# Kernel optimization log

Hardware: AMD Instinct MI355X
Metric: run time of the kernel (lower is better)

The kernel has to match this reference:

```python
import jax, jax.numpy as jnp
import numpy as np

HID = 64; N_LAYERS = 4; N_HEADS = 4; HEAD_DIM = 16; INTER = 32; MAXP = 1024; EPS = 1e-12


def setup_inputs() -> dict:
    key = jax.random.key(0)
    ks = iter(jax.random.split(key, 32))
    rn = lambda shape, s=0.02: jax.random.normal(next(ks), shape, jnp.float32) * s
    B, L = 32, 1024
    return {
        "features": jax.random.normal(next(ks), (B, L, HID), jnp.float32),
        "Wq": rn((N_LAYERS, HID, HID)), "bq": jnp.zeros((N_LAYERS, HID), jnp.float32),
        "Wk": rn((N_LAYERS, HID, HID)), "bk": jnp.zeros((N_LAYERS, HID), jnp.float32),
        "Wv": rn((N_LAYERS, HID, HID)), "bv": jnp.zeros((N_LAYERS, HID), jnp.float32),
        "Wo": rn((N_LAYERS, HID, HID)), "bo": jnp.zeros((N_LAYERS, HID), jnp.float32),
        "ln1_g": jnp.ones((N_LAYERS, HID), jnp.float32), "ln1_b": jnp.zeros((N_LAYERS, HID), jnp.float32),
        "Wi": rn((N_LAYERS, HID, INTER)), "bi": jnp.zeros((N_LAYERS, INTER), jnp.float32),
        "Wd": rn((N_LAYERS, INTER, HID)), "bd": jnp.zeros((N_LAYERS, HID), jnp.float32),
        "ln2_g": jnp.ones((N_LAYERS, HID), jnp.float32), "ln2_b": jnp.zeros((N_LAYERS, HID), jnp.float32),
        "rel_emb": rn((N_LAYERS, 2 * MAXP - 1, HEAD_DIM)),
        "fc_w": rn((HID, 6)), "fc_b": jnp.zeros((6,), jnp.float32),
    }


def _ln(x, g, b):
    m = jnp.mean(x, axis=-1, keepdims=True)
    v = jnp.mean((x - m) ** 2, axis=-1, keepdims=True)
    return (x - m) / jnp.sqrt(v + EPS) * g + b


def reference(features, Wq, bq, Wk, bk, Wv, bv, Wo, bo, ln1_g, ln1_b,
              Wi, bi, Wd, bd, ln2_g, ln2_b, rel_emb, fc_w, fc_b):
    B, L, _ = features.shape
    pos = jnp.arange(L)
    dist_idx = pos[:, None] - pos[None, :] + (MAXP - 1)  # [L, L] in [0, 2*MAXP-2]
    scale = np.float32(1.0 / np.sqrt(HEAD_DIM))

    def heads(t):  # [B,L,HID] -> [B,H,L,D]
        return t.reshape(B, L, N_HEADS, HEAD_DIM).transpose(0, 2, 1, 3)

    x = features
    for i in range(N_LAYERS):
        q = heads(x @ Wq[i] + bq[i])
        k = heads(x @ Wk[i] + bk[i])
        v = heads(x @ Wv[i] + bv[i])
        scores = jnp.einsum("bhld,bhrd->bhlr", q, k)
        pe = rel_emb[i][dist_idx]  # [L, L, D] relative_key positional embedding
        scores = scores + jnp.einsum("bhld,lrd->bhlr", q, pe)
        probs = jax.nn.softmax(scores * scale, axis=-1)
        ctx = jnp.einsum("bhlr,bhrd->bhld", probs, v).transpose(0, 2, 1, 3).reshape(B, L, HID)
        x = _ln(ctx @ Wo[i] + bo[i] + x, ln1_g[i], ln1_b[i])
        inter = jax.nn.gelu(x @ Wi[i] + bi[i], approximate=False)
        x = _ln(inter @ Wd[i] + bd[i] + x, ln2_g[i], ln2_b[i])
    return (x @ fc_w + fc_b)[:, 1:, :]
```

## Files before the change

### kernel.cpp

```cpp
#include <hip/hip_runtime.h>
#include <math.h>

static constexpr int Bc = 32;
static constexpr int Lc = 1024;

typedef _Float16 f16x4 __attribute__((ext_vector_type(4)));
typedef __fp16   h16x2 __attribute__((ext_vector_type(2)));
typedef float    f32x4 __attribute__((ext_vector_type(4)));

#define MFMA16(a, b, c) __builtin_amdgcn_mfma_f32_16x16x16f16((a), (b), (c), 0, 0, 0)

#if __has_builtin(__builtin_amdgcn_exp2f)
#define EXP2(x) __builtin_amdgcn_exp2f(x)
#else
#define EXP2(x) exp2f(x)
#endif

__global__ __launch_bounds__(256) void prep_kernel(
    const float* __restrict__ features, const float* __restrict__ rel,
    const float* __restrict__ Wq, const float* __restrict__ Wk,
    const float* __restrict__ Wv, const float* __restrict__ Wo,
    const float* __restrict__ Wi, const float* __restrict__ Wd,
    _Float16* __restrict__ xh, _Float16* __restrict__ relh,
    _Float16* __restrict__ wt)
{
    int i = blockIdx.x * 256 + threadIdx.x;
    {
        float4 v = ((const float4*)features)[i];
        h16x2 a = __builtin_amdgcn_cvt_pkrtz(v.x, v.y);
        h16x2 b = __builtin_amdgcn_cvt_pkrtz(v.z, v.w);
        f16x4 o; o[0] = a[0]; o[1] = a[1]; o[2] = b[0]; o[3] = b[1];
        ((f16x4*)xh)[i] = o;
    }
    if (i < 32752) {
        float4 v = ((const float4*)rel)[i];
        h16x2 a = __builtin_amdgcn_cvt_pkrtz(v.x, v.y);
        h16x2 b = __builtin_amdgcn_cvt_pkrtz(v.z, v.w);
        f16x4 o; o[0] = a[0]; o[1] = a[1]; o[2] = b[0]; o[3] = b[1];
        ((f16x4*)relh)[i] = o;
    }
    if (i < 65536) {
        int which = i >> 14, r = i & 16383;
        int m = r >> 12, k = (r >> 6) & 63, c = r & 63;
        const float* src = which == 0 ? Wq : which == 1 ? Wk : which == 2 ? Wv : Wo;
        wt[which * 16384 + m * 4096 + c * 64 + k] = (_Float16)src[r];
    } else if (i < 73728) {
        int r = i - 65536;
        int m = r >> 11, k = (r >> 5) & 63, c = r & 31;
        wt[65536 + m * 2048 + c * 64 + k] = (_Float16)Wi[r];
    } else if (i < 81920) {
        int r = i - 73728;
        int m = r >> 11, k = (r >> 6) & 31, c = r & 63;
        wt[73728 + m * 2048 + c * 32 + k] = (_Float16)Wd[r];
    }
}

__global__ __launch_bounds__(256) void qkv_kernel(
    const _Float16* __restrict__ xh,
    const _Float16* __restrict__ qT, const _Float16* __restrict__ kT,
    const _Float16* __restrict__ vT,
    const float* __restrict__ bq, const float* __restrict__ bk,
    const float* __restrict__ bv,
    _Float16* __restrict__ qo, _Float16* __restrict__ ko, _Float16* __restrict__ vt)
{
    const int t = threadIdx.x, wv = t >> 6, lane = t & 63, lo = lane & 15, hi = lane >> 4;
    const int row0 = blockIdx.x * 64 + wv * 16;
    const int b = row0 >> 10, l0 = row0 & 1023;

    f16x4 a[4];
    #pragma unroll
    for (int kk = 0; kk < 4; kk++)
        a[kk] = *(const f16x4*)(xh + (row0 + lo) * 64 + kk * 16 + 4 * hi);

    #pragma unroll
    for (int m = 0; m < 3; m++) {
        const _Float16* WT = m == 0 ? qT : m == 1 ? kT : vT;
        const float* bias  = m == 0 ? bq : m == 1 ? bk : bv;
        #pragma unroll
        for (int h = 0; h < 4; h++) {
            float bb = bias[h * 16 + lo];
            f32x4 acc = { bb, bb, bb, bb };
            #pragma unroll
            for (int kk = 0; kk < 4; kk++) {
                f16x4 bf = *(const f16x4*)(WT + (h * 16 + lo) * 64 + kk * 16 + 4 * hi);
                acc = MFMA16(a[kk], bf, acc);
            }
            int bh = b * 4 + h;
            if (m < 2) {
                _Float16* dst = (m == 0 ? qo : ko) + (bh * Lc + l0 + 4 * hi) * 16 + lo;
                dst[0]  = (_Float16)acc[0];
                dst[16] = (_Float16)acc[1];
                dst[32] = (_Float16)acc[2];
                dst[48] = (_Float16)acc[3];
            } else {
                h16x2 p0 = __builtin_amdgcn_cvt_pkrtz(acc[0], acc[1]);
                h16x2 p1 = __builtin_amdgcn_cvt_pkrtz(acc[2], acc[3]);
                f16x4 o; o[0] = p0[0]; o[1] = p0[1]; o[2] = p1[0]; o[3] = p1[1];
                *(f16x4*)(vt + (bh * 16 + lo) * Lc + l0 + 4 * hi) = o;
            }
        }
    }
}

__global__ __launch_bounds__(64) void attn_kernel(
    const _Float16* __restrict__ qg, const _Float16* __restrict__ kg,
    const _Float16* __restrict__ vtg, const _Float16* __restrict__ relh,
    _Float16* __restrict__ ctxh)
{
    __shared__ float Tl[4][16 * 52];
    const int lane = threadIdx.x & 63;
    const int bh = blockIdx.x >> 4;
    const int l0 = (blockIdx.x & 15) * 64;
    const int lo = lane & 15, hi = lane >> 4;

    const _Float16 qscale = (_Float16)0.36067376022224085f;
    f16x4 qf[4];
    #pragma unroll
    for (int i = 0; i < 4; i++) {
        qf[i] = *(const f16x4*)(qg + (bh * Lc + l0 + 16 * i + lo) * 16 + 4 * hi);
        #pragma unroll
        for (int j = 0; j < 4; j++) qf[i][j] *= qscale;
    }

    const int o = 12 + lo - 4 * hi;

    float* wrE[4]; float* wrO[4]; const float* rdE[4]; const float* rdO[4];
    #pragma unroll
    for (int i = 0; i < 4; i++) {
        float* ring = Tl[i];
        const int phiE = 16 * (i & 1);
        const int phiO = 16 - phiE;
        wrE[i] = ring + lo * 52 + phiE + 4 * hi;
        wrO[i] = ring + lo * 52 + phiO + 4 * hi;
        rdE[i] = ring + lo * 52 + phiE + o;
        rdO[i] = ring + lo * 52 + phiO + o;
    }

    const _Float16* rbase = relh + 4 * hi;
    auto ldrel = [&](int row) {
        row = row > 2046 ? 2046 : row;
        return *(const f16x4*)(rbase + row * 16);
    };
    auto t_store = [&](f16x4 rf, f16x4 q, float* wr, bool mir) {
        f32x4 z = { 0.f, 0.f, 0.f, 0.f };
        f32x4 tt = MFMA16(rf, q, z);
        *(f32x4*)(wr) = tt;
        if (mir) *(f32x4*)(wr + 32) = tt;
    };

    f16x4 P[6];
    #pragma unroll
    for (int k = 0; k < 6; k++) P[k] = ldrel(l0 + 16 * k + lo);
    #pragma unroll
    for (int i = 0; i < 4; i++) {
        t_store(P[i],     qf[i], wrE[i], (i & 1) == 0);
        t_store(P[i + 1], qf[i], wrO[i], (i & 1) == 1);
    }
    f16x4 rc0 = P[2], rc1 = P[3], rc2 = P[4], rc3 = P[5];
    int rrow = l0 + 96 + lo;

    const _Float16* kp = kg  + (bh * Lc + 1008 + lo) * 16 + 4 * hi;
    const _Float16* vp = vtg + (bh * 16 + lo) * Lc + 1008 + 4 * hi;
    f16x4 kfc = *(const f16x4*)kp;
    f16x4 vfc = *(const f16x4*)vp;

    f32x4 ot[4], d[4];
    #pragma unroll
    for (int i = 0; i < 4; i++) {
        ot[i] = f32x4{ 0.f, 0.f, 0.f, 0.f };
        d[i]  = f32x4{ 0.f, 0.f, 0.f, 0.f };
    }

    #pragma unroll 2
    for (int t = 0; t < 64; ++t) {
        kp -= 256; vp -= 16;
        f16x4 kfn = *(const f16x4*)kp;
        f16x4 vfn = *(const f16x4*)vp;
        f16x4 r4 = ldrel(rrow); rrow += 16;

        f32x4 s[4];
        #pragma unroll
        for (int i = 0; i < 4; i++) {
            const float* rd = (t & 1) ? rdO[i] : rdE[i];
            f32x4 si;
            si[0] = rd[3]; si[1] = rd[2]; si[2] = rd[1]; si[3] = rd[0];
            s[i] = MFMA16(kfc, qf[i], si);
        }

        float e[4][4];
        #pragma unroll
        for (int i = 0; i < 4; i++)
            #pragma unroll
            for (int j = 0; j < 4; j++) {
                e[i][j] = EXP2(s[i][j]);
                d[i][j] += e[i][j];
            }

        t_store(rc0, qf[0], (t & 1) ? wrO[0] : wrE[0], (t & 1) == 0);
        t_store(rc1, qf[1], (t & 1) ? wrO[1] : wrE[1], (t & 1) == 1);
        t_store(rc2, qf[2], (t & 1) ? wrO[2] : wrE[2], (t & 1) == 0);
        t_store(rc3, qf[3], (t & 1) ? wrO[3] : wrE[3], (t & 1) == 1);

        #pragma unroll
        for (int i = 0; i < 4; i++) {
            h16x2 pa = __builtin_amdgcn_cvt_pkrtz(e[i][0], e[i][1]);
            h16x2 pb = __builtin_amdgcn_cvt_pkrtz(e[i][2], e[i][3]);
            f16x4 pf; pf[0] = pa[0]; pf[1] = pa[1]; pf[2] = pb[0]; pf[3] = pb[1];
            ot[i] = MFMA16(vfc, pf, ot[i]);
        }

        kfc = kfn; vfc = vfn;
        rc0 = rc1; rc1 = rc2; rc2 = rc3; rc3 = r4;
    }

    const int b = bh >> 2, h = bh & 3;
    #pragma unroll
    for (int i = 0; i < 4; i++) {
        float den = (d[i][0] + d[i][1]) + (d[i][2] + d[i][3]);
        den += __shfl_xor(den, 16);
        den += __shfl_xor(den, 32);
        const float inv = 1.f / den;
        h16x2 o0 = __builtin_amdgcn_cvt_pkrtz(ot[i][0] * inv, ot[i][1] * inv);
        h16x2 o1 = __builtin_amdgcn_cvt_pkrtz(ot[i][2] * inv, ot[i][3] * inv);
        f16x4 o4; o4[0] = o0[0]; o4[1] = o0[1]; o4[2] = o1[0]; o4[3] = o1[1];
        *(f16x4*)(ctxh + (b * Lc + l0 + 16 * i + lo) * 64 + h * 16 + 4 * hi) = o4;
    }
}

__global__ __launch_bounds__(256) void tail_kernel(
    const _Float16* __restrict__ ctxh, const float* __restrict__ resid,
    const _Float16* __restrict__ woT, const float* __restrict__ bo,
    const float* __restrict__ g1, const float* __restrict__ b1,
    const _Float16* __restrict__ wiT, const float* __restrict__ bi,
    const _Float16* __restrict__ wdT, const float* __restrict__ bd,
    const float* __restrict__ g2, const float* __restrict__ b2,
    float* __restrict__ xout,
    int doq,
    const _Float16* __restrict__ qT, const _Float16* __restrict__ kT,
    const _Float16* __restrict__ vT,
    const float* __restrict__ bq, const float* __restrict__ bk,
    const float* __restrict__ bv,
    _Float16* __restrict__ qo, _Float16* __restrict__ ko, _Float16* __restrict__ vt)
{
    __shared__ _Float16 x1s[4][16 * 68];
    __shared__ _Float16 ins[4][16 * 36];
    const int t = threadIdx.x, wv = t >> 6, lane = t & 63, lo = lane & 15, hi = lane >> 4;
    const int row0 = blockIdx.x * 64 + wv * 16;

    f16x4 a[4];
    #pragma unroll
    for (int kk = 0; kk < 4; kk++)
        a[kk] = *(const f16x4*)(ctxh + (row0 + lo) * 64 + kk * 16 + 4 * hi);

    float c1[4][4];
    #pragma unroll
    for (int w = 0; w < 4; w++) {
        float bb = bo[w * 16 + lo];
        f32x4 acc;
        #pragma unroll
        for (int j = 0; j < 4; j++)
            acc[j] = bb + resid[(row0 + 4 * hi + j) * 64 + w * 16 + lo];
        #pragma unroll
        for (int kk = 0; kk < 4; kk++) {
            f16x4 bf = *(const f16x4*)(woT + (w * 16 + lo) * 64 + kk * 16 + 4 * hi);
            acc = MFMA16(a[kk], bf, acc);
        }
        #pragma unroll
        for (int j = 0; j < 4; j++) c1[w][j] = acc[j];
    }

    float x1[4][4];
    {
        float gg[4], bb2[4];
        #pragma unroll
        for (int w = 0; w < 4; w++) { gg[w] = g1[w * 16 + lo]; bb2[w] = b1[w * 16 + lo]; }
        #pragma unroll
        for (int j = 0; j < 4; j++) {
            float s = c1[0][j] + c1[1][j] + c1[2][j] + c1[3][j];
            float q = c1[0][j]*c1[0][j] + c1[1][j]*c1[1][j] + c1[2][j]*c1[2][j] + c1[3][j]*c1[3][j];
            #pragma unroll
            for (int off = 1; off < 16; off <<= 1) { s += __shfl_xor(s, off); q += __shfl_xor(q, off); }
            float m  = s * (1.f / 64.f);
            float vr = q * (1.f / 64.f) - m * m;
            float rs = rsqrtf(vr + 1e-12f);
            #pragma unroll
            for (int w = 0; w < 4; w++) x1[w][j] = (c1[w][j] - m) * rs * gg[w] + bb2[w];
        }
    }

    _Float16* xsp = x1s[wv];
    #pragma unroll
    for (int w = 0; w < 4; w++)
        #pragma unroll
        for (int j = 0; j < 4; j++)
            xsp[(4 * hi + j) * 68 + w * 16 + lo] = (_Float16)x1[w][j];
    f16x4 a2[4];
    #pragma unroll
    for (int kk = 0; kk < 4; kk++)
        a2[kk] = *(const f16x4*)(xsp + lo * 68 + kk * 16 + 4 * hi);

    float it[2][4];
    #pragma unroll
    for (int w = 0; w < 2; w++) {
        float bb = bi[w * 16 + lo];
        f32x4 acc = { bb, bb, bb, bb };
        #pragma unroll
        for (int kk = 0; kk < 4; kk++) {
            f16x4 bf = *(const f16x4*)(wiT + (w * 16 + lo) * 64 + kk * 16 + 4 * hi);
            acc = MFMA16(a2[kk], bf, acc);
        }
        #pragma unroll
        for (int j = 0; j < 4; j++) {
            float v = acc[j];
            it[w][j] = 0.5f * v * (1.f + erff(v * 0.70710678118654752f));
        }
    }

    _Float16* isp = ins[wv];
    #pragma unroll
    for (int w = 0; w < 2; w++)
        #pragma unroll
        for (int j = 0; j < 4; j++)
            isp[(4 * hi + j) * 36 + w * 16 + lo] = (_Float16)it[w][j];
    f16x4 a3[2];
    #pragma unroll
    for (int kk = 0; kk < 2; kk++)
        a3[kk] = *(const f16x4*)(isp + lo * 36 + kk * 16 + 4 * hi);

    float c2[4][4];
    #pragma unroll
    for (int w = 0; w < 4; w++) {
        float bb = bd[w * 16 + lo];
        f32x4 acc;
        #pragma unroll
        for (int j = 0; j < 4; j++) acc[j] = bb + x1[w][j];
        #pragma unroll
        for (int kk = 0; kk < 2; kk++) {
            f16x4 bf = *(const f16x4*)(wdT + (w * 16 + lo) * 32 + kk * 16 + 4 * hi);
            acc = MFMA16(a3[kk], bf, acc);
        }
        #pragma unroll
        for (int j = 0; j < 4; j++) c2[w][j] = acc[j];
    }

    float x2[4][4];
    {
        float gg[4], bb2[4];
        #pragma unroll
        for (int w = 0; w < 4; w++) { gg[w] = g2[w * 16 + lo]; bb2[w] = b2[w * 16 + lo]; }
        #pragma unroll
        for (int j = 0; j < 4; j++) {
            float s = c2[0][j] + c2[1][j] + c2[2][j] + c2[3][j];
            float q = c2[0][j]*c2[0][j] + c2[1][j]*c2[1][j] + c2[2][j]*c2[2][j] + c2[3][j]*c2[3][j];
            #pragma unroll
            for (int off = 1; off < 16; off <<= 1) { s += __shfl_xor(s, off); q += __shfl_xor(q, off); }
            float m  = s * (1.f / 64.f);
            float vr = q * (1.f / 64.f) - m * m;
            float rs = rsqrtf(vr + 1e-12f);
            #pragma unroll
            for (int w = 0; w < 4; w++) {
                float xv = (c2[w][j] - m) * rs * gg[w] + bb2[w];
                x2[w][j] = xv;
                xout[(row0 + 4 * hi + j) * 64 + w * 16 + lo] = xv;
            }
        }
    }

    if (!doq) return;

    #pragma unroll
    for (int w = 0; w < 4; w++)
        #pragma unroll
        for (int j = 0; j < 4; j++)
            xsp[(4 * hi + j) * 68 + w * 16 + lo] = (_Float16)x2[w][j];
    f16x4 aq[4];
    #pragma unroll
    for (int kk = 0; kk < 4; kk++)
        aq[kk] = *(const f16x4*)(xsp + lo * 68 + kk * 16 + 4 * hi);

    const int b = row0 >> 10, l0q = row0 & 1023;
    #pragma unroll
    for (int m = 0; m < 3; m++) {
        const _Float16* WT = m == 0 ? qT : m == 1 ? kT : vT;
        const float* bias  = m == 0 ? bq : m == 1 ? bk : bv;
        #pragma unroll
        for (int h = 0; h < 4; h++) {
            float bb = bias[h * 16 + lo];
            f32x4 acc = { bb, bb, bb, bb };
            #pragma unroll
            for (int kk = 0; kk < 4; kk++) {
                f16x4 bf = *(const f16x4*)(WT + (h * 16 + lo) * 64 + kk * 16 + 4 * hi);
                acc = MFMA16(aq[kk], bf, acc);
            }
            int bh = b * 4 + h;
            if (m < 2) {
                _Float16* dst = (m == 0 ? qo : ko) + (bh * Lc + l0q + 4 * hi) * 16 + lo;
                dst[0]  = (_Float16)acc[0];
                dst[16] = (_Float16)acc[1];
                dst[32] = (_Float16)acc[2];
                dst[48] = (_Float16)acc[3];
            } else {
                h16x2 p0 = __builtin_amdgcn_cvt_pkrtz(acc[0], acc[1]);
                h16x2 p1 = __builtin_amdgcn_cvt_pkrtz(acc[2], acc[3]);
                f16x4 o; o[0] = p0[0]; o[1] = p0[1]; o[2] = p1[0]; o[3] = p1[1];
                *(f16x4*)(vt + (bh * 16 + lo) * Lc + l0q + 4 * hi) = o;
            }
        }
    }
}

__global__ __launch_bounds__(256) void final_kernel(
    const float* __restrict__ x, const float* __restrict__ fcw,
    const float* __restrict__ fcb, float* __restrict__ out)
{
    int idx = blockIdx.x * 256 + threadIdx.x;
    if (idx >= Bc * 1023 * 6) return;
    int j = idx % 6;
    int rest = idx / 6;
    int l = rest % 1023 + 1;
    int b = rest / 1023;
    const float* xr = x + (b * Lc + l) * 64;
    float acc = fcb[j];
    for (int k = 0; k < 64; ++k) acc += xr[k] * fcw[k * 6 + j];
    out[idx] = acc;
}

extern "C" void kernel_launch(void* const* d_in, const int* in_sizes, int n_in,
                              void* d_out, int out_size, void* d_ws, size_t ws_size,
                              hipStream_t stream)
{
    (void)in_sizes; (void)n_in; (void)out_size; (void)ws_size;
    const float* features = (const float*)d_in[0];
    const float* Wq  = (const float*)d_in[1];
    const float* bq  = (const float*)d_in[2];
    const float* Wk  = (const float*)d_in[3];
    const float* bk  = (const float*)d_in[4];
    const float* Wv  = (const float*)d_in[5];
    const float* bv  = (const float*)d_in[6];
    const float* Wo  = (const float*)d_in[7];
    const float* bo  = (const float*)d_in[8];
    const float* g1  = (const float*)d_in[9];
    const float* b1  = (const float*)d_in[10];
    const float* Wi  = (const float*)d_in[11];
    const float* bi  = (const float*)d_in[12];
    const float* Wd  = (const float*)d_in[13];
    const float* bd  = (const float*)d_in[14];
    const float* g2  = (const float*)d_in[15];
    const float* b2  = (const float*)d_in[16];
    const float* rel = (const float*)d_in[17];
    const float* fcw = (const float*)d_in[18];
    const float* fcb = (const float*)d_in[19];
    float* out = (float*)d_out;

    char* ws = (char*)d_ws;
    float*    xbuf = (float*)(ws);
    _Float16* xh   = (_Float16*)(ws + ( 8u << 20));
    _Float16* ctxh = (_Float16*)(ws + (12u << 20));
    _Float16* qh   = (_Float16*)(ws + (16u << 20));
    _Float16* kh   = (_Float16*)(ws + (20u << 20));
    _Float16* vt   = (_Float16*)(ws + (24u << 20));
    _Float16* relh = (_Float16*)(ws + (28u << 20));
    _Float16* wt   = (_Float16*)(ws + (28u << 20) + (512u << 10));

    prep_kernel<<<2048, 256, 0, stream>>>(features, rel, Wq, Wk, Wv, Wo, Wi, Wd,
                                          xh, relh, wt);
    qkv_kernel<<<512, 256, 0, stream>>>(xh,
        wt, wt + 16384, wt + 32768, bq, bk, bv, qh, kh, vt);

    for (int i = 0; i < 4; ++i) {
        const float* resid = (i == 0) ? features : xbuf;
        int ni = i + 1;
        attn_kernel<<<2048, 64, 0, stream>>>(qh, kh, vt,
            relh + i * 2047 * 16, ctxh);
        tail_kernel<<<512, 256, 0, stream>>>(ctxh, resid,
            wt + 49152 + i * 4096, bo + i * 64, g1 + i * 64, b1 + i * 64,
            wt + 65536 + i * 2048, bi + i * 32,
            wt + 73728 + i * 2048, bd + i * 64, g2 + i * 64, b2 + i * 64,
            xbuf,
            (i < 3) ? 1 : 0,
            wt + ni * 4096, wt + 16384 + ni * 4096, wt + 32768 + ni * 4096,
            bq + ni * 64, bk + ni * 64, bv + ni * 64,
            qh, kh, vt);
    }
    final_kernel<<<768, 256, 0, stream>>>(xbuf, fcw, fcb, out);
}
```

Measured before the change: 288.4 us.

## Deepen K/V prefetch, prefetch relative-score LDS reads, and remap block order

After: 299.3 us. +3.8%, slower.

```diff
diff --git a/kernel.cpp b/kernel.cpp
--- a/kernel.cpp
+++ b/kernel.cpp
@@ -109,8 +109,8 @@
 {
     __shared__ float Tl[4][16 * 52];
     const int lane = threadIdx.x & 63;
-    const int bh = blockIdx.x >> 4;
-    const int l0 = (blockIdx.x & 15) * 64;
+    const int bh = blockIdx.x & 127;
+    const int l0 = (blockIdx.x >> 7) * 64;
     const int lo = lane & 15, hi = lane >> 4;
 
     const _Float16 qscale = (_Float16)0.36067376022224085f;
@@ -159,10 +159,20 @@
     f16x4 rc0 = P[2], rc1 = P[3], rc2 = P[4], rc3 = P[5];
     int rrow = l0 + 96 + lo;
 
+    f32x4 si[4];
+    #pragma unroll
+    for (int i = 0; i < 4; i++) {
+        const float* rd = rdE[i];
+        si[i][0] = rd[3]; si[i][1] = rd[2]; si[i][2] = rd[1]; si[i][3] = rd[0];
+    }
+
     const _Float16* kp = kg  + (bh * Lc + 1008 + lo) * 16 + 4 * hi;
     const _Float16* vp = vtg + (bh * 16 + lo) * Lc + 1008 + 4 * hi;
-    f16x4 kfc = *(const f16x4*)kp;
-    f16x4 vfc = *(const f16x4*)vp;
+    f16x4 kf0 = *(const f16x4*)kp;
+    f16x4 vf0 = *(const f16x4*)vp;
+    kp -= 256; vp -= 16;
+    f16x4 kf1 = *(const f16x4*)kp;
+    f16x4 vf1 = *(const f16x4*)vp;
 
     f32x4 ot[4], d[4];
     #pragma unroll
@@ -174,18 +184,14 @@
     #pragma unroll 2
     for (int t = 0; t < 64; ++t) {
         kp -= 256; vp -= 16;
-        f16x4 kfn = *(const f16x4*)kp;
-        f16x4 vfn = *(const f16x4*)vp;
+        f16x4 kf2 = *(const f16x4*)kp;
+        f16x4 vf2 = *(const f16x4*)vp;
         f16x4 r4 = ldrel(rrow); rrow += 16;
 
         f32x4 s[4];
         #pragma unroll
-        for (int i = 0; i < 4; i++) {
-            const float* rd = (t & 1) ? rdO[i] : rdE[i];
-            f32x4 si;
-            si[0] = rd[3]; si[1] = rd[2]; si[2] = rd[1]; si[3] = rd[0];
-            s[i] = MFMA16(kfc, qf[i], si);
-        }
+        for (int i = 0; i < 4; i++)
+            s[i] = MFMA16(kf0, qf[i], si[i]);
 
         float e[4][4];
         #pragma unroll
@@ -203,13 +209,20 @@
 
         #pragma unroll
         for (int i = 0; i < 4; i++) {
+            const float* rd = (t & 1) ? rdE[i] : rdO[i];
+            si[i][0] = rd[3]; si[i][1] = rd[2]; si[i][2] = rd[1]; si[i][3] = rd[0];
+        }
+
+        #pragma unroll
+        for (int i = 0; i < 4; i++) {
             h16x2 pa = __builtin_amdgcn_cvt_pkrtz(e[i][0], e[i][1]);
             h16x2 pb = __builtin_amdgcn_cvt_pkrtz(e[i][2], e[i][3]);
             f16x4 pf; pf[0] = pa[0]; pf[1] = pa[1]; pf[2] = pb[0]; pf[3] = pb[1];
-            ot[i] = MFMA16(vfc, pf, ot[i]);
-        }
-
-        kfc = kfn; vfc = vfn;
+            ot[i] = MFMA16(vf0, pf, ot[i]);
+        }
+
+        kf0 = kf1; kf1 = kf2;
+        vf0 = vf1; vf1 = vf2;
         rc0 = rc1; rc1 = rc2; rc2 = rc3; rc3 = r4;
     }
 
```
